# Optimization experiments

Hardware: AMD Instinct MI355X
Metric: run time of the kernel (lower is better)

The kernel has to match this reference:

```python
import jax, jax.numpy as jnp
import numpy as np

D = 4096; K = 512; HOP = 512; WIN = 16384
NUM_REGIONS = 1 + (WIN - D) // HOP            # 25
D2_Y = 128; K2 = 128; STRIDE_Y = 2
D3_X = 25; K3 = 256
NR2Y = 1 + (K - D2_Y) // STRIDE_Y             # 193
NR3X = 1 + (NUM_REGIONS - D3_X)               # 1
M = 128


def create_filters(d=D, k=K, sr=44100, start_freq=50, end_freq=6000):
    x = jnp.linspace(0.0, 2 * np.pi, d + 1)[:d]
    num_cycles = start_freq * d / sr
    scaling_ind = np.log(end_freq / start_freq) / k
    window_mask = 1.0 - jnp.cos(x)
    phases = jnp.exp(jnp.arange(float(k)) * scaling_ind)[None, :] * num_cycles * x[:, None]
    filters = jnp.stack((jnp.cos(phases), jnp.sin(phases)), axis=2) * window_mask[:, None, None]
    return filters.astype(jnp.float32)          # [d, k, 2]


def setup_inputs() -> dict:
    key = jax.random.key(0)
    k1, k2, k3, k4 = jax.random.split(key, 4)
    x = jax.random.normal(k1, (128, WIN), dtype=jnp.float32)
    filters = create_filters().reshape(D, 2 * K)                     # [4096, 1024]
    # Conv weights in OIHW layout (torch Conv2d convention), kaiming-ish scale
    conv1_w = jax.random.normal(k2, (K2, 1, 1, D2_Y), dtype=jnp.float32) / np.sqrt(D2_Y)
    conv2_w = jax.random.normal(k3, (K3, K2, D3_X, 1), dtype=jnp.float32) / np.sqrt(K2 * D3_X)
    beta_w = jax.random.normal(k4, (M, NR3X * NR2Y * K3), dtype=jnp.float32) / np.sqrt(NR3X * NR2Y * K3)
    return {"x": x, "filters": filters, "conv1_w": conv1_w, "conv2_w": conv2_w, "beta_w": beta_w}


def reference(x, filters, conv1_w, conv2_w, beta_w):
    B = x.shape[0]
    # unfold(1, D, HOP): overlapping windows -> [B, NUM_REGIONS, D]
    idx = jnp.arange(NUM_REGIONS)[:, None] * HOP + jnp.arange(D)[None, :]
    windows = x[:, idx]                                               # [B, 25, 4096]
    spec = windows @ filters                                          # [B, 25, 1024]
    # complex magnitude^2: pairs of (cos, sin) components
    zx = jnp.sum(spec.reshape(B, NUM_REGIONS, K, 2) ** 2, axis=3)     # [B, 25, 512]
    zx = jnp.log(zx + 1e-14)[:, None]                                 # [B, 1, 25, 512]
    dn = ("NCHW", "OIHW", "NCHW")
    h = jax.lax.conv_general_dilated(zx, conv1_w, (1, STRIDE_Y), "VALID", dimension_numbers=dn)
    h = jax.nn.relu(h)                                                # [B, 128, 25, 193]
    h = jax.lax.conv_general_dilated(h, conv2_w, (1, 1), "VALID", dimension_numbers=dn)
    h = jax.nn.relu(h)                                                # [B, 256, 1, 193]
    y = h.reshape(B, -1) @ beta_w.T                                   # [B, 128]
    return y
```

## Files before the change

### kernel.cpp

```cpp
#include <hip/hip_runtime.h>
#include <hip/hip_bf16.h>
#include <math.h>


typedef __attribute__((ext_vector_type(8))) short s8v;
typedef __attribute__((ext_vector_type(8))) _Float16 half8;
typedef __attribute__((ext_vector_type(16))) float f16v;

__device__ inline ushort f2bf(float f) {
    union { float f; unsigned u; } v; v.f = f;
    unsigned u = v.u;
    return (ushort)((u + 0x7FFFu + ((u >> 16) & 1u)) >> 16);
}

__global__ void k0x_xh(const float* __restrict__ x, _Float16* __restrict__ xh) {
    int i = blockIdx.x * 256 + threadIdx.x;
    xh[i] = (_Float16)x[i];
}

__global__ __launch_bounds__(256)
void k0f_fB(const float* __restrict__ filt, _Float16* __restrict__ fB) {
    __shared__ float tile[8][257];
    const int t   = threadIdx.x;
    const int n0  = blockIdx.x * 256;
    const int kc8 = blockIdx.y;
    for (int idx = t; idx < 8 * 256; idx += 256) {
        int kk = idx >> 8, n = idx & 255;
        tile[kk][n] = filt[(kc8 * 8 + kk) * 1024 + n0 + n];
    }
    __syncthreads();
    half8 v;
#pragma unroll
    for (int j = 0; j < 8; j++) v[j] = (_Float16)tile[j][t];
    *(half8*)(fB + (size_t)kc8 * 8192 + (size_t)(n0 + t) * 8) = v;
}

__global__ void k0a_w1b(const float* __restrict__ w1, ushort* __restrict__ w1b) {
    int i = blockIdx.x * 256 + threadIdx.x;
    w1b[i] = f2bf(w1[i]);
}

__global__ void k0b_w2c(const float* __restrict__ w2, ushort* __restrict__ w2c) {
    int i = blockIdx.x * 256 + threadIdx.x;
    int k2 = i & 127;
    int dx = (i >> 7) % 25;
    int k3 = i / 3200;
    w2c[i] = f2bf(w2[(k3 * 128 + k2) * 25 + dx]);
}

__global__ void k0c_bb(const float* __restrict__ beta, ushort* __restrict__ bb) {
    int i = blockIdx.x * 256 + threadIdx.x;
    bb[i] = f2bf(beta[i]);
}

#define K1P(KB, LP, VU, VL, RL, RW, DOPREF, DOWRITE)                               \
  {                                                                                \
    asm volatile("s_waitcnt lgkmcnt(0)" ::: "memory");                             \
    __builtin_amdgcn_s_barrier();                                                  \
    asm volatile("" ::: "memory");                                                 \
    if (DOPREF) {                                                                  \
      RL[0] = *(const half8*)(apt + ((KB) + 2) * 32);                              \
      RL[1] = *(const half8*)(apt + ((KB) + 2) * 32 + 16);                         \
      _Pragma("unroll")                                                            \
      for (int s = 0; s < 2; s++) {                                                \
        const _Float16* pBk = pB + ((size_t)((KB) + 2) * 2 + s) * 16384;           \
        VL[s][0] = *(const half8*)(pBk);                                           \
        VL[s][1] = *(const half8*)(pBk + 256);                                     \
      }                                                                            \
    }                                                                              \
    _Pragma("unroll")                                                              \
    for (int s = 0; s < 2; s++) {                                                  \
      half8 a0 = *(const half8*)((const char*)Al + (LP) * 8192 + s * 4096 +        \
                                 (wm + ml) * 32 + qf * 16);                        \
      half8 a1 = *(const half8*)((const char*)Al + (LP) * 8192 + s * 4096 +        \
                                 (wm + 32 + ml) * 32 + qf * 16);                   \
      acc[0][0] = __builtin_amdgcn_mfma_f32_32x32x16_f16(a0, VU[s][0], acc[0][0], 0, 0, 0); \
      acc[0][1] = __builtin_amdgcn_mfma_f32_32x32x16_f16(a0, VU[s][1], acc[0][1], 0, 0, 0); \
      acc[1][0] = __builtin_amdgcn_mfma_f32_32x32x16_f16(a1, VU[s][0], acc[1][0], 0, 0, 0); \
      acc[1][1] = __builtin_amdgcn_mfma_f32_32x32x16_f16(a1, VU[s][1], acc[1][1], 0, 0, 0); \
    }                                                                              \
    if (DOWRITE) {                                                                 \
      half8* dnx = (half8*)((char*)Al + (1 - (LP)) * 8192);                        \
      dnx[t] = RW[0];                                                              \
      dnx[256 + t] = RW[1];                                                        \
    }                                                                              \
  }

__global__ __launch_bounds__(256)
void k1_mfma(const _Float16* __restrict__ xh, const _Float16* __restrict__ fB,
             ushort* __restrict__ zxb) {
    __shared__ _Float16 Al[2][4096];
    const int t  = threadIdx.x;
    const int n0 = blockIdx.x * 128;
    const int m0 = blockIdx.y * 128;
    const int w  = t >> 6, l = t & 63;
    const int wm = (w >> 1) * 64, wn = (w & 1) * 64;
    const int qf = l >> 5;
    const int ml = l & 31;

    const int srow = t >> 1;
    const int sq   = t & 1;
    const int gm   = m0 + srow;
    const _Float16* apt = xh + (gm / 25) * 16384 + (gm % 25) * 512 + sq * 8;

    const _Float16* pB = fB + ((size_t)qf * 1024 + (size_t)(n0 + wn + ml)) * 8;

    f16v acc[2][2];
#pragma unroll
    for (int i = 0; i < 2; i++)
#pragma unroll
        for (int j = 0; j < 2; j++)
#pragma unroll
            for (int r = 0; r < 16; r++) acc[i][j][r] = 0.f;

    half8 vb0[2][2], vb1[2][2], vb2[2][2], vb3[2][2];
    half8 rA0[2], rA1[2];

    {
        rA0[0] = *(const half8*)(apt);
        rA0[1] = *(const half8*)(apt + 16);
        half8* d0 = (half8*)Al;
        d0[t] = rA0[0];
        d0[256 + t] = rA0[1];
        rA1[0] = *(const half8*)(apt + 32);
        rA1[1] = *(const half8*)(apt + 48);
#pragma unroll
        for (int s = 0; s < 2; s++) {
            const _Float16* pBk = pB + (size_t)s * 16384;
            vb0[s][0] = *(const half8*)(pBk);
            vb0[s][1] = *(const half8*)(pBk + 256);
            const _Float16* pBk1 = pB + ((size_t)2 + s) * 16384;
            vb1[s][0] = *(const half8*)(pBk1);
            vb1[s][1] = *(const half8*)(pBk1 + 256);
        }
    }

    for (int it = 0; it < 31; it++) {
        const int kb = it * 4;
        K1P(kb + 0, 0, vb0, vb2, rA0, rA1, true, true)
        K1P(kb + 1, 1, vb1, vb3, rA1, rA0, true, true)
        K1P(kb + 2, 0, vb2, vb0, rA0, rA1, true, true)
        K1P(kb + 3, 1, vb3, vb1, rA1, rA0, true, true)
    }
    K1P(124, 0, vb0, vb2, rA0, rA1, true, true)
    K1P(125, 1, vb1, vb3, rA1, rA0, true, true)
    K1P(126, 0, vb2, vb0, rA0, rA1, false, true)
    K1P(127, 1, vb3, vb1, rA1, rA0, false, false)

#pragma unroll
    for (int mt = 0; mt < 2; mt++)
#pragma unroll
        for (int nt = 0; nt < 2; nt++) {
#pragma unroll
            for (int r = 0; r < 16; r++) {
                float val = acc[mt][nt][r];
                float oth = __shfl_xor(val, 1, 64);
                if (!(l & 1)) {
                    float pw = fmaf(val, val, fmaf(oth, oth, 1e-14f));
                    int m = m0 + wm + mt * 32 + 4 * qf + (r & 3) + 8 * (r >> 2);
                    int n = n0 + wn + nt * 32 + ml;
                    zxb[m * 512 + (n >> 1)] = f2bf(logf(pw));
                }
            }
        }
}

#define ZPITCH 272
__global__ __launch_bounds__(256, 2)
void k2_mfma(const ushort* __restrict__ zxb, const ushort* __restrict__ w1b,
             const ushort* __restrict__ w2c, ushort* __restrict__ h2b) {
    __shared__ ushort zl[2 * 3 * 4 * ZPITCH];
    __shared__ ushort h1l[3 * 16 * 64 * 8];
    const int t  = threadIdx.x;
    const int yt = blockIdx.x;
    const int b  = blockIdx.y;
    const int y0 = yt * 64;
    const int w  = t >> 6;
    const int l  = t & 63;
    const int yy = l & 31;
    const int q  = l >> 5;

    s8v w1f[8];
    {
        const ushort* wp = w1b + (32 * w + yy) * 128 + 8 * q;
#pragma unroll
        for (int ks = 0; ks < 8; ks++)
            w1f[ks] = *(const s8v*)(wp + 16 * ks);
    }

    f16v acc[2][2];
#pragma unroll
    for (int mt = 0; mt < 2; mt++)
#pragma unroll
        for (int nt = 0; nt < 2; nt++)
#pragma unroll
            for (int r = 0; r < 16; r++) acc[mt][nt][r] = 0.f;

    {
        const int nq = 3 * 4 * 62;
        for (int idx = t; idx < nq; idx += 256) {
            int iq = idx % 62;
            int dc = idx / 62;
            int c = dc & 3, d = dc >> 2;
            const ushort* src = zxb + ((b * 25 + d) << 9);
            int gg = 2 * y0 + 2 * c + 4 * iq;
            ushort* dst = zl + (d * 4 + c) * ZPITCH + 4 * iq;
#pragma unroll
            for (int u = 0; u < 4; u++) {
                int g = gg + u;
                dst[u] = (g < 512) ? src[g] : (ushort)0;
            }
        }
    }

    for (int ch = 0; ch < 9; ch++) {
        const int p  = ch & 1;
        const int nd = (ch == 8) ? 1 : 3;
        __syncthreads();

        ushort pv[12];
        int nq2 = 0;
        if (ch < 8) {
            const int nd2 = (ch == 7) ? 1 : 3;
            nq2 = nd2 * 4 * 62;
#pragma unroll
            for (int r = 0; r < 3; r++) {
                int idx = t + r * 256;
                if (idx < nq2) {
                    int iq = idx % 62;
                    int dc = idx / 62;
                    int c = dc & 3, d = dc >> 2;
                    const ushort* src = zxb + ((b * 25 + (ch + 1) * 3 + d) << 9);
                    int gg = 2 * y0 + 2 * c + 4 * iq;
#pragma unroll
                    for (int u = 0; u < 4; u++) {
                        int g = gg + u;
                        pv[r * 4 + u] = (g < 512) ? src[g] : (ushort)0;
                    }
                }
            }
        }

        for (int d = 0; d < nd; d++) {
            const int zb = (p * 3 + d) * 4;
#pragma unroll
            for (int nt = 0; nt < 2; nt++) {
                const int ye = nt * 32 + yy;
                const ushort* zp = zl + (zb + (ye & 3)) * ZPITCH + 8 * (ye >> 2) + 8 * q;
                f16v a1;
#pragma unroll
                for (int r = 0; r < 16; r++) a1[r] = 0.f;
#pragma unroll
                for (int ks = 0; ks < 8; ks++) {
                    s8v bf = *(const s8v*)(zp + 16 * ks);
                    a1 = __builtin_amdgcn_mfma_f32_32x32x16_bf16(w1f[ks], bf, a1, 0, 0, 0);
                }
#pragma unroll
                for (int g = 0; g < 4; g++) {
                    unsigned p0 = (unsigned)f2bf(fmaxf(a1[4 * g + 0], 0.f))
                                | ((unsigned)f2bf(fmaxf(a1[4 * g + 1], 0.f)) << 16);
                    unsigned p1 = (unsigned)f2bf(fmaxf(a1[4 * g + 2], 0.f))
                                | ((unsigned)f2bf(fmaxf(a1[4 * g + 3], 0.f)) << 16);
                    unsigned* dst = (unsigned*)(h1l + (((d * 16 + 4 * w + g) * 64) + ye) * 8 + 4 * q);
                    dst[0] = p0; dst[1] = p1;
                }
            }
        }

        if (ch < 8) {
#pragma unroll
            for (int r = 0; r < 3; r++) {
                int idx = t + r * 256;
                if (idx < nq2) {
                    int iq = idx % 62;
                    int dc = idx / 62;
                    int c = dc & 3, d = dc >> 2;
                    ushort* dst = zl + (((1 - p) * 3 + d) * 4 + c) * ZPITCH + 4 * iq;
#pragma unroll
                    for (int u = 0; u < 4; u++) dst[u] = pv[r * 4 + u];
                }
            }
        }

        __syncthreads();

        for (int d = 0; d < nd; d++) {
            const int dxa = ch * 3 + d;
            const ushort* ap = w2c + (size_t)(64 * w + yy) * 3200 + dxa * 128 + 8 * q;
#pragma unroll
            for (int ks = 0; ks < 8; ks++) {
                s8v a0 = *(const s8v*)(ap + 16 * ks);
                s8v a1f = *(const s8v*)(ap + (size_t)32 * 3200 + 16 * ks);
#pragma unroll
                for (int nt = 0; nt < 2; nt++) {
                    s8v hb = *(const s8v*)(h1l + (((d * 16 + 2 * ks + q) * 64) + nt * 32 + yy) * 8);
                    acc[0][nt] = __builtin_amdgcn_mfma_f32_32x32x16_bf16(a0, hb, acc[0][nt], 0, 0, 0);
                    acc[1][nt] = __builtin_amdgcn_mfma_f32_32x32x16_bf16(a1f, hb, acc[1][nt], 0, 0, 0);
                }
            }
        }
    }

#pragma unroll
    for (int mt = 0; mt < 2; mt++)
#pragma unroll
        for (int nt = 0; nt < 2; nt++) {
            int y = y0 + nt * 32 + yy;
            if (y < 193) {
#pragma unroll
                for (int r = 0; r < 16; r++) {
                    int k3 = 64 * w + 32 * mt + (r & 3) + 8 * (r >> 2) + 4 * q;
                    h2b[(b * 256 + k3) * 193 + y] = f2bf(fmaxf(acc[mt][nt][r], 0.f));
                }
            }
        }
}

__global__ __launch_bounds__(256)
void k4_mfma(const ushort* __restrict__ h2b, const ushort* __restrict__ bb,
             float* __restrict__ part) {
    const int t = threadIdx.x, w = t >> 6, l = t & 63;
    const int s = blockIdx.x;
    const int kb = s * 256;
    const int qf = l >> 5;
    const int ml = l & 31;
    const ushort* pa  = h2b + (size_t)(w * 32 + ml) * 49408 + kb + qf * 8;
    const ushort* pb0 = bb  + (size_t)ml * 49408 + kb + qf * 8;

    f16v acc[4];
#pragma unroll
    for (int nt = 0; nt < 4; nt++)
#pragma unroll
        for (int r = 0; r < 16; r++) acc[nt][r] = 0.f;

    for (int ks = 0; ks < 16; ks++) {
        s8v af = *(const s8v*)(pa + ks * 16);
#pragma unroll
        for (int nt = 0; nt < 4; nt++) {
            s8v bf = *(const s8v*)(pb0 + (size_t)nt * 32 * 49408 + ks * 16);
            acc[nt] = __builtin_amdgcn_mfma_f32_32x32x16_bf16(af, bf, acc[nt], 0, 0, 0);
        }
    }
    float* pp = part + (size_t)s * 16384;
#pragma unroll
    for (int nt = 0; nt < 4; nt++)
#pragma unroll
        for (int r = 0; r < 16; r++) {
            int m = w * 32 + 4 * qf + (r & 3) + 8 * (r >> 2);
            pp[m * 128 + nt * 32 + ml] = acc[nt][r];
        }
}

__global__ __launch_bounds__(256)
void k5_red(const float* __restrict__ part, float* __restrict__ out) {
    __shared__ float red[256];
    const int t  = threadIdx.x;
    const int io = t & 63;
    const int kq = t >> 6;
    const int i  = blockIdx.x * 64 + io;
    float s = 0.f;
#pragma unroll 4
    for (int k = kq; k < 193; k += 4) s += part[(size_t)k * 16384 + i];
    red[t] = s;
    __syncthreads();
    if (t < 64)
        out[blockIdx.x * 64 + t] = (red[t] + red[t + 64]) + (red[t + 128] + red[t + 192]);
}

extern "C" void kernel_launch(void* const* d_in, const int* in_sizes, int n_in,
                              void* d_out, int out_size, void* d_ws, size_t ws_size,
                              hipStream_t stream) {
    const float* x    = (const float*)d_in[0];
    const float* filt = (const float*)d_in[1];
    const float* w1   = (const float*)d_in[2];
    const float* w2   = (const float*)d_in[3];
    const float* beta = (const float*)d_in[4];
    float* out = (float*)d_out;

    char* ws = (char*)d_ws;
    ushort*   zxb  = (ushort*)(ws + 0);
    ushort*   h2b  = (ushort*)(ws + 3276800);
    ushort*   w1b  = (ushort*)(ws + 15921152);
    ushort*   w2c  = (ushort*)(ws + 15953920);
    ushort*   bb   = (ushort*)(ws + 17592320);
    _Float16* xh   = (_Float16*)(ws + 30240768);
    _Float16* fB   = (_Float16*)(ws + 34435072);
    float*    part = (float*)(ws + 30240768);

    k0x_xh<<<8192, 256, 0, stream>>>(x, xh);
    k0f_fB<<<dim3(4, 512), 256, 0, stream>>>(filt, fB);
    k0a_w1b<<<64, 256, 0, stream>>>(w1, w1b);
    k0b_w2c<<<3200, 256, 0, stream>>>(w2, w2c);
    k0c_bb<<<24704, 256, 0, stream>>>(beta, bb);
    k1_mfma<<<dim3(8, 25), 256, 0, stream>>>(xh, fB, zxb);
    k2_mfma<<<dim3(4, 128), 256, 0, stream>>>(zxb, w1b, w2c, h2b);
    k4_mfma<<<193, 256, 0, stream>>>(h2b, bb, part);
    k5_red<<<256, 256, 0, stream>>>(part, out);
}
```

Measured before the change: 293.9 us.

## Fuse preprocessing conversions into one kernel, swap k1 grid order, prefetch k2 weights

Merges the five separate fp32-to-half/bf16 conversion kernels into a single grid-stride kernel to cut launch overhead. The k1 GEMM grid is transposed so consecutive blocks walk the M (row) dimension, which changes L2 reuse of the filter tiles. In k2 the conv2 weight fragments are double-buffered in registers, so the next chunk loads while MFMAs run. The fused kernel loses the shared-memory transpose for the filter layout and uses strided reads instead, and the register prefetch raises register pressure.

```diff
diff --git a/kernel.cpp b/kernel.cpp
--- a/kernel.cpp
+++ b/kernel.cpp
@@ -13,44 +13,43 @@
     return (ushort)((u + 0x7FFFu + ((u >> 16) & 1u)) >> 16);
 }
 
-__global__ void k0x_xh(const float* __restrict__ x, _Float16* __restrict__ xh) {
-    int i = blockIdx.x * 256 + threadIdx.x;
-    xh[i] = (_Float16)x[i];
-}
-
+#define K0_E0 2097152
+#define K0_E1 2621440
+#define K0_E2 2637824
+#define K0_E3 3457024
+#define K0_E4 9781248
 __global__ __launch_bounds__(256)
-void k0f_fB(const float* __restrict__ filt, _Float16* __restrict__ fB) {
-    __shared__ float tile[8][257];
-    const int t   = threadIdx.x;
-    const int n0  = blockIdx.x * 256;
-    const int kc8 = blockIdx.y;
-    for (int idx = t; idx < 8 * 256; idx += 256) {
-        int kk = idx >> 8, n = idx & 255;
-        tile[kk][n] = filt[(kc8 * 8 + kk) * 1024 + n0 + n];
-    }
-    __syncthreads();
-    half8 v;
-#pragma unroll
-    for (int j = 0; j < 8; j++) v[j] = (_Float16)tile[j][t];
-    *(half8*)(fB + (size_t)kc8 * 8192 + (size_t)(n0 + t) * 8) = v;
-}
-
-__global__ void k0a_w1b(const float* __restrict__ w1, ushort* __restrict__ w1b) {
-    int i = blockIdx.x * 256 + threadIdx.x;
-    w1b[i] = f2bf(w1[i]);
-}
-
-__global__ void k0b_w2c(const float* __restrict__ w2, ushort* __restrict__ w2c) {
-    int i = blockIdx.x * 256 + threadIdx.x;
-    int k2 = i & 127;
-    int dx = (i >> 7) % 25;
-    int k3 = i / 3200;
-    w2c[i] = f2bf(w2[(k3 * 128 + k2) * 25 + dx]);
-}
-
-__global__ void k0c_bb(const float* __restrict__ beta, ushort* __restrict__ bb) {
-    int i = blockIdx.x * 256 + threadIdx.x;
-    bb[i] = f2bf(beta[i]);
+void k0all(const float* __restrict__ x, const float* __restrict__ filt,
+           const float* __restrict__ w1, const float* __restrict__ w2,
+           const float* __restrict__ beta,
+           _Float16* __restrict__ xh, _Float16* __restrict__ fB,
+           ushort* __restrict__ w1b, ushort* __restrict__ w2c,
+           ushort* __restrict__ bb) {
+    for (int i = blockIdx.x * 256 + threadIdx.x; i < K0_E4; i += gridDim.x * 256) {
+        if (i < K0_E0) {
+            xh[i] = (_Float16)x[i];
+        } else if (i < K0_E1) {
+            int o = i - K0_E0;
+            int kc8 = o >> 10, nn = o & 1023;
+            const float* fp = filt + (size_t)(kc8 * 8) * 1024 + nn;
+            half8 v;
+#pragma unroll
+            for (int j = 0; j < 8; j++) v[j] = (_Float16)fp[(size_t)j * 1024];
+            *(half8*)(fB + (size_t)o * 8) = v;
+        } else if (i < K0_E2) {
+            int o = i - K0_E1;
+            w1b[o] = f2bf(w1[o]);
+        } else if (i < K0_E3) {
+            int o = i - K0_E2;
+            int k2 = o & 127;
+            int dx = (o >> 7) % 25;
+            int k3 = o / 3200;
+            w2c[o] = f2bf(w2[(k3 * 128 + k2) * 25 + dx]);
+        } else {
+            int o = i - K0_E3;
+            bb[o] = f2bf(beta[o]);
+        }
+    }
 }
 
 #define K1P(KB, LP, VU, VL, RL, RW, DOPREF, DOWRITE)                               \
@@ -91,8 +90,8 @@
              ushort* __restrict__ zxb) {
     __shared__ _Float16 Al[2][4096];
     const int t  = threadIdx.x;
-    const int n0 = blockIdx.x * 128;
-    const int m0 = blockIdx.y * 128;
+    const int n0 = blockIdx.y * 128;
+    const int m0 = blockIdx.x * 128;
     const int w  = t >> 6, l = t & 63;
     const int wm = (w >> 1) * 64, wn = (w & 1) * 64;
     const int qf = l >> 5;
@@ -284,18 +283,44 @@
 
         __syncthreads();
 
-        for (int d = 0; d < nd; d++) {
-            const int dxa = ch * 3 + d;
-            const ushort* ap = w2c + (size_t)(64 * w + yy) * 3200 + dxa * 128 + 8 * q;
-#pragma unroll
-            for (int ks = 0; ks < 8; ks++) {
-                s8v a0 = *(const s8v*)(ap + 16 * ks);
-                s8v a1f = *(const s8v*)(ap + (size_t)32 * 3200 + 16 * ks);
-#pragma unroll
-                for (int nt = 0; nt < 2; nt++) {
-                    s8v hb = *(const s8v*)(h1l + (((d * 16 + 2 * ks + q) * 64) + nt * 32 + yy) * 8);
-                    acc[0][nt] = __builtin_amdgcn_mfma_f32_32x32x16_bf16(a0, hb, acc[0][nt], 0, 0, 0);
-                    acc[1][nt] = __builtin_amdgcn_mfma_f32_32x32x16_bf16(a1f, hb, acc[1][nt], 0, 0, 0);
+        {
+            const ushort* apb = w2c + (size_t)(64 * w + yy) * 3200 + (ch * 3) * 128 + 8 * q;
+            s8v afA[4][2], afB[4][2];
+#pragma unroll
+            for (int ks = 0; ks < 4; ks++) {
+                afA[ks][0] = *(const s8v*)(apb + 16 * ks);
+                afA[ks][1] = *(const s8v*)(apb + (size_t)32 * 3200 + 16 * ks);
+            }
+            for (int d = 0; d < nd; d++) {
+                const ushort* ap  = apb + d * 128;
+                const ushort* apn = apb + ((d + 1 < nd) ? (d + 1) : d) * 128;
+#pragma unroll
+                for (int ks = 0; ks < 4; ks++) {
+                    afB[ks][0] = *(const s8v*)(ap + 64 + 16 * ks);
+                    afB[ks][1] = *(const s8v*)(ap + (size_t)32 * 3200 + 64 + 16 * ks);
+                }
+#pragma unroll
+                for (int ks = 0; ks < 4; ks++) {
+#pragma unroll
+                    for (int nt = 0; nt < 2; nt++) {
+                        s8v hb = *(const s8v*)(h1l + (((d * 16 + 2 * ks + q) * 64) + nt * 32 + yy) * 8);
+                        acc[0][nt] = __builtin_amdgcn_mfma_f32_32x32x16_bf16(afA[ks][0], hb, acc[0][nt], 0, 0, 0);
+                        acc[1][nt] = __builtin_amdgcn_mfma_f32_32x32x16_bf16(afA[ks][1], hb, acc[1][nt], 0, 0, 0);
+                    }
+                }
+#pragma unroll
+                for (int ks = 0; ks < 4; ks++) {
+                    afA[ks][0] = *(const s8v*)(apn + 16 * ks);
+                    afA[ks][1] = *(const s8v*)(apn + (size_t)32 * 3200 + 16 * ks);
+                }
+#pragma unroll
+                for (int ks = 0; ks < 4; ks++) {
+#pragma unroll
+                    for (int nt = 0; nt < 2; nt++) {
+                        s8v hb = *(const s8v*)(h1l + (((d * 16 + 2 * (ks + 4) + q) * 64) + nt * 32 + yy) * 8);
+                        acc[0][nt] = __builtin_amdgcn_mfma_f32_32x32x16_bf16(afB[ks][0], hb, acc[0][nt], 0, 0, 0);
+                        acc[1][nt] = __builtin_amdgcn_mfma_f32_32x32x16_bf16(afB[ks][1], hb, acc[1][nt], 0, 0, 0);
+                    }
                 }
             }
         }
@@ -387,12 +412,8 @@
     _Float16* fB   = (_Float16*)(ws + 34435072);
     float*    part = (float*)(ws + 30240768);
 
-    k0x_xh<<<8192, 256, 0, stream>>>(x, xh);
-    k0f_fB<<<dim3(4, 512), 256, 0, stream>>>(filt, fB);
-    k0a_w1b<<<64, 256, 0, stream>>>(w1, w1b);
-    k0b_w2c<<<3200, 256, 0, stream>>>(w2, w2c);
-    k0c_bb<<<24704, 256, 0, stream>>>(beta, bb);
-    k1_mfma<<<dim3(8, 25), 256, 0, stream>>>(xh, fB, zxb);
+    k0all<<<2048, 256, 0, stream>>>(x, filt, w1, w2, beta, xh, fB, w1b, w2c, bb);
+    k1_mfma<<<dim3(25, 8), 256, 0, stream>>>(xh, fB, zxb);
     k2_mfma<<<dim3(4, 128), 256, 0, stream>>>(zxb, w1b, w2c, h2b);
     k4_mfma<<<193, 256, 0, stream>>>(h2b, bb, part);
     k5_red<<<256, 256, 0, stream>>>(part, out);
```

Measured after the change: 300.6 us. 1.02x slower.
